# Kernel tuning notes

Measured on AMD Instinct MI355X. Metric: run time of the kernel, lower is better.

## Reference

```python
import jax, jax.numpy as jnp
import numpy as np

NUM_CLUSTERS = 512
EMBED_DIM = 256
BATCH = 65536
ALPHA = 0.05

def setup_inputs() -> dict:
    key = jax.random.key(0)
    k1, k2 = jax.random.split(key)
    embeddings = jax.random.normal(k1, (BATCH, EMBED_DIM), dtype=jnp.float32)
    # torch.randn centers drawn inside forward; materialized here for determinism
    centers = jax.random.normal(k2, (NUM_CLUSTERS, EMBED_DIM), dtype=jnp.float32)
    return {"embeddings": embeddings, "centers": centers}

def reference(embeddings, centers):
    # the broadcast difference, without the huge [N, K, D] intermediate).
    x_sq = jnp.sum(embeddings * embeddings, axis=1, keepdims=True)      # [N, 1]
    c_sq = jnp.sum(centers * centers, axis=1)[None, :]                  # [1, K]
    cross = embeddings @ centers.T                                      # [N, K]
    distances = jnp.sqrt(jnp.maximum(x_sq + c_sq - 2.0 * cross, 0.0))   # [N, K]
    cluster_assignments = jnp.argmin(distances, axis=1)                 # [N] int
    # gather distance to assigned (nearest) center
    cluster_loss = jnp.take_along_axis(
        distances, cluster_assignments[:, None], axis=1)[:, 0]          # [N]
    kmeans_loss = jnp.mean(cluster_loss)
    return kmeans_loss * ALPHA
```

## Files before the change

kernel.cpp:

```cpp
#include <hip/hip_runtime.h>
#include <hip/hip_bf16.h>

#define NROWS 65536
#define DIM   256
#define KC    512
#define ALPHA 0.05f

#define BM   64
#define SLD  264

typedef __attribute__((ext_vector_type(8))) short bf16x8;
typedef __attribute__((ext_vector_type(4))) float f32x4;

static __device__ __forceinline__ unsigned short f2bf(float f) {
    union { __hip_bfloat16 h; unsigned short u; } c;
    c.h = __float2bfloat16(f);
    return c.u;
}
static __device__ __forceinline__ float bf2f(unsigned short u) {
    union { unsigned short u; __hip_bfloat16 h; } c;
    c.u = u;
    return __bfloat162float(c.h);
}

__global__ void prep_centers(const float* __restrict__ centers,
                             float* __restrict__ csqh,
                             uint4* __restrict__ cbf2,
                             float* __restrict__ out) {
    const int t = threadIdx.x;
    const int r = blockIdx.x * 8 + (t >> 5);
    const int e = t & 31;
    const float4* cv = reinterpret_cast<const float4*>(centers);
    float4 v0 = cv[r * 64 + e * 2];
    float4 v1 = cv[r * 64 + e * 2 + 1];
    float s = v0.x * v0.x + v0.y * v0.y + v0.z * v0.z + v0.w * v0.w
            + v1.x * v1.x + v1.y * v1.y + v1.z * v1.z + v1.w * v1.w;
    unsigned short o[8];
    o[0] = f2bf(v0.x); o[1] = f2bf(v0.y); o[2] = f2bf(v0.z); o[3] = f2bf(v0.w);
    o[4] = f2bf(v1.x); o[5] = f2bf(v1.y); o[6] = f2bf(v1.z); o[7] = f2bf(v1.w);
    const int ch = r >> 6, w = (r >> 4) & 3, m = r & 15;
    const int kk = e >> 2, q = e & 3, l = q * 16 + m;
    cbf2[(((ch * 4 + w) * 8) + kk) * 64 + l] = *reinterpret_cast<uint4*>(o);
    #pragma unroll
    for (int off = 16; off; off >>= 1) s += __shfl_xor(s, off, 64);
    if (e == 0) csqh[r] = 0.5f * s;
    if (blockIdx.x == 0 && t == 0) out[0] = 0.f;
}

__global__ __launch_bounds__(256, 2) void kmeans_main(
    const float* __restrict__ emb,
    const uint4* __restrict__ cbf2,
    const float* __restrict__ csqh_g,
    float* __restrict__ out) {
    __shared__ unsigned short sA[BM * SLD];
    __shared__ float xsq_s[BM];
    __shared__ float rowmax_s[4][BM];

    const int t = threadIdx.x;
    const int w = t >> 6;
    const int lane = t & 63;
    const int m = lane & 15;
    const int q = lane >> 4;
    const int row0 = blockIdx.x * BM;

    const float4* embv = reinterpret_cast<const float4*>(emb + (size_t)row0 * DIM);
    #pragma unroll
    for (int i = 0; i < 16; ++i) {
        int f = t + 256 * i;
        int r = f >> 6;
        int c4 = f & 63;
        float4 v = embv[r * 64 + c4];
        ushort4 o;
        o.x = f2bf(v.x); o.y = f2bf(v.y); o.z = f2bf(v.z); o.w = f2bf(v.w);
        *reinterpret_cast<ushort4*>(&sA[r * SLD + c4 * 4]) = o;
    }
    __syncthreads();

    {
        int r = w * 16 + (lane >> 2);
        int qq = lane & 3;
        const ushort4* p = reinterpret_cast<const ushort4*>(&sA[r * SLD + qq * 64]);
        float s = 0.f;
        #pragma unroll
        for (int j = 0; j < 16; ++j) {
            ushort4 u = p[j];
            float a = bf2f(u.x), b = bf2f(u.y), c = bf2f(u.z), d = bf2f(u.w);
            s += a * a + b * b + c * c + d * d;
        }
        s += __shfl_xor(s, 1, 64);
        s += __shfl_xor(s, 2, 64);
        if (qq == 0) xsq_s[r] = s;
    }

    bf16x8 afr[4][8];
    #pragma unroll
    for (int rt = 0; rt < 4; ++rt)
        #pragma unroll
        for (int k = 0; k < 8; ++k)
            afr[rt][k] = *reinterpret_cast<const bf16x8*>(
                &sA[(rt * 16 + m) * SLD + k * 32 + q * 8]);

    float c2h[8];
    #pragma unroll
    for (int ch = 0; ch < 8; ++ch) c2h[ch] = csqh_g[ch * 64 + w * 16 + m];

    float maxv[4][4];
    #pragma unroll
    for (int rt = 0; rt < 4; ++rt)
        #pragma unroll
        for (int rg = 0; rg < 4; ++rg) maxv[rt][rg] = -1e30f;

    const bf16x8* cb2 = reinterpret_cast<const bf16x8*>(cbf2);

    bf16x8 bcur[8];
    #pragma unroll
    for (int kk = 0; kk < 8; ++kk)
        bcur[kk] = cb2[((0 * 4 + w) * 8 + kk) * 64 + lane];

    #pragma unroll
    for (int ch = 0; ch < 8; ++ch) {
        bf16x8 bnxt[8];
        if (ch < 7) {
            #pragma unroll
            for (int kk = 0; kk < 8; ++kk)
                bnxt[kk] = cb2[(((ch + 1) * 4 + w) * 8 + kk) * 64 + lane];
        }
        const float ci = -c2h[ch];
        f32x4 acc[4];
        #pragma unroll
        for (int rt = 0; rt < 4; ++rt) acc[rt] = (f32x4){ci, ci, ci, ci};
        #pragma unroll
        for (int kk = 0; kk < 8; ++kk)
            #pragma unroll
            for (int rt = 0; rt < 4; ++rt)
                acc[rt] = __builtin_amdgcn_mfma_f32_16x16x32_bf16(
                    afr[rt][kk], bcur[kk], acc[rt], 0, 0, 0);
        #pragma unroll
        for (int rt = 0; rt < 4; ++rt)
            #pragma unroll
            for (int rg = 0; rg < 4; ++rg)
                maxv[rt][rg] = fmaxf(maxv[rt][rg], acc[rt][rg]);
        if (ch < 7) {
            #pragma unroll
            for (int kk = 0; kk < 8; ++kk) bcur[kk] = bnxt[kk];
        }
    }

    #pragma unroll
    for (int rt = 0; rt < 4; ++rt)
        #pragma unroll
        for (int rg = 0; rg < 4; ++rg) {
            float v = maxv[rt][rg];
            v = fmaxf(v, __shfl_xor(v, 1, 64));
            v = fmaxf(v, __shfl_xor(v, 2, 64));
            v = fmaxf(v, __shfl_xor(v, 4, 64));
            v = fmaxf(v, __shfl_xor(v, 8, 64));
            if (m == 0) rowmax_s[w][rt * 16 + q * 4 + rg] = v;
        }
    __syncthreads();

    if (t < 64) {
        float M = fmaxf(fmaxf(rowmax_s[0][t], rowmax_s[1][t]),
                        fmaxf(rowmax_s[2][t], rowmax_s[3][t]));
        float d = sqrtf(fmaxf(xsq_s[t] - 2.f * M, 0.f));
        #pragma unroll
        for (int off = 1; off < 64; off <<= 1) d += __shfl_xor(d, off, 64);
        if (t == 0) atomicAdd(out, d * (ALPHA / (float)NROWS));
    }
}

extern "C" void kernel_launch(void* const* d_in, const int* in_sizes, int n_in,
                              void* d_out, int out_size, void* d_ws, size_t ws_size,
                              hipStream_t stream) {
    const float* emb     = (const float*)d_in[0];
    const float* centers = (const float*)d_in[1];
    float* out = (float*)d_out;

    float* csqh = (float*)d_ws;
    uint4* cbf2 = (uint4*)((char*)d_ws + 2048);

    prep_centers<<<dim3(KC / 8), dim3(256), 0, stream>>>(centers, csqh, cbf2, out);
    kmeans_main<<<dim3(NROWS / BM), dim3(256), 0, stream>>>(emb, cbf2, csqh, out);
}
```

Measured before the change: 118.9 us.

## Make kmeans blocks persistent over four tiles with double-buffered direct-to-LDS loads

Each block now handles four 64-row tiles instead of one. Embedding rows are staged as fp32 in two LDS buffers using global_load_lds DMA, and the next tile's rows are issued between MFMA chunks so global loads overlap compute. Conversion to bf16 and the squared-norm computation move to the fragment-load stage. Occupancy drops to one block per CU because fp32 double buffers use much more LDS, and the correctness of the manual waitcnt/barrier synchronisation is delicate.

```diff
diff --git a/kernel.cpp b/kernel.cpp
--- a/kernel.cpp
+++ b/kernel.cpp
@@ -6,8 +6,10 @@
 #define KC    512
 #define ALPHA 0.05f
 
-#define BM   64
-#define SLD  264
+#define BM    64
+#define NT    4
+#define GRID  (NROWS / (BM * NT))
+#define SROW  260
 
 typedef __attribute__((ext_vector_type(8))) short bf16x8;
 typedef __attribute__((ext_vector_type(4))) float f32x4;
@@ -47,126 +49,148 @@
     if (blockIdx.x == 0 && t == 0) out[0] = 0.f;
 }
 
-__global__ __launch_bounds__(256, 2) void kmeans_main(
+__global__ __launch_bounds__(256, 1) void kmeans_main(
     const float* __restrict__ emb,
     const uint4* __restrict__ cbf2,
     const float* __restrict__ csqh_g,
     float* __restrict__ out) {
-    __shared__ unsigned short sA[BM * SLD];
-    __shared__ float xsq_s[BM];
-    __shared__ float rowmax_s[4][BM];
+    __shared__ __align__(16) float fbuf[2][BM * SROW];
+    __shared__ float xsq_s[2][4][BM];
+    __shared__ float rowmax_s[2][4][BM];
 
     const int t = threadIdx.x;
     const int w = t >> 6;
     const int lane = t & 63;
     const int m = lane & 15;
     const int q = lane >> 4;
-    const int row0 = blockIdx.x * BM;
-
-    const float4* embv = reinterpret_cast<const float4*>(emb + (size_t)row0 * DIM);
-    #pragma unroll
-    for (int i = 0; i < 16; ++i) {
-        int f = t + 256 * i;
-        int r = f >> 6;
-        int c4 = f & 63;
-        float4 v = embv[r * 64 + c4];
-        ushort4 o;
-        o.x = f2bf(v.x); o.y = f2bf(v.y); o.z = f2bf(v.z); o.w = f2bf(v.w);
-        *reinterpret_cast<ushort4*>(&sA[r * SLD + c4 * 4]) = o;
+    const size_t block_row0 = (size_t)blockIdx.x * (BM * NT);
+
+    float c2h[8];
+    #pragma unroll
+    for (int ch = 0; ch < 8; ++ch) c2h[ch] = csqh_g[ch * 64 + w * 16 + m];
+
+    const bf16x8* cb2 = reinterpret_cast<const bf16x8*>(cbf2);
+
+#define DMA_ROW(tt_, bb_, rr_)                                                   \
+    do {                                                                         \
+        const float* g_ = emb +                                                  \
+            (block_row0 + (size_t)(tt_) * BM + (size_t)(rr_)) * DIM + (lane << 2); \
+        __builtin_amdgcn_global_load_lds(                                        \
+            (const __attribute__((address_space(1))) void*)g_,                   \
+            (__attribute__((address_space(3))) void*)&fbuf[bb_][(rr_) * SROW],   \
+            16, 0, 0);                                                           \
+    } while (0)
+
+    #pragma unroll
+    for (int j = 0; j < 16; ++j) DMA_ROW(0, 0, w * 16 + j);
+    #pragma unroll
+    for (int j = 0; j < 16; ++j) DMA_ROW(1, 1, w * 16 + j);
+    asm volatile("s_waitcnt vmcnt(16)\n\ts_barrier" ::: "memory");
+
+    for (int tt = 0; tt < NT; ++tt) {
+        const int p = tt & 1;
+        const bool dma_on = (tt + 2 < NT);
+
+        bf16x8 afr[4][8];
+        float xacc[4] = {0.f, 0.f, 0.f, 0.f};
+        #pragma unroll
+        for (int rt = 0; rt < 4; ++rt) {
+            const float* rp = &fbuf[p][(rt * 16 + m) * SROW + q * 8];
+            #pragma unroll
+            for (int kk = 0; kk < 8; ++kk) {
+                f32x4 v0 = *reinterpret_cast<const f32x4*>(rp + kk * 32);
+                f32x4 v1 = *reinterpret_cast<const f32x4*>(rp + kk * 32 + 4);
+                unsigned short o[8];
+                o[0] = f2bf(v0.x); o[1] = f2bf(v0.y); o[2] = f2bf(v0.z); o[3] = f2bf(v0.w);
+                o[4] = f2bf(v1.x); o[5] = f2bf(v1.y); o[6] = f2bf(v1.z); o[7] = f2bf(v1.w);
+                afr[rt][kk] = *reinterpret_cast<bf16x8*>(o);
+                if ((kk >> 1) == w) {
+                    #pragma unroll
+                    for (int j = 0; j < 8; ++j) { float f = bf2f(o[j]); xacc[rt] += f * f; }
+                }
+            }
+        }
+        #pragma unroll
+        for (int rt = 0; rt < 4; ++rt) {
+            float s = xacc[rt];
+            s += __shfl_xor(s, 16, 64);
+            s += __shfl_xor(s, 32, 64);
+            if (q == 0) xsq_s[p][w][rt * 16 + m] = s;
+        }
+
+        bf16x8 bcur[8];
+        #pragma unroll
+        for (int kk = 0; kk < 8; ++kk)
+            bcur[kk] = cb2[((0 * 4 + w) * 8 + kk) * 64 + lane];
+
+        asm volatile("s_waitcnt lgkmcnt(0)\n\ts_barrier" ::: "memory");
+
+        float maxv[4][4];
+        #pragma unroll
+        for (int rt = 0; rt < 4; ++rt)
+            #pragma unroll
+            for (int rg = 0; rg < 4; ++rg) maxv[rt][rg] = -1e30f;
+
+        #pragma unroll
+        for (int ch = 0; ch < 8; ++ch) {
+            if (dma_on) {
+                DMA_ROW(tt + 2, p, w * 16 + 2 * ch);
+                DMA_ROW(tt + 2, p, w * 16 + 2 * ch + 1);
+            }
+            bf16x8 bnxt[8];
+            if (ch < 7) {
+                #pragma unroll
+                for (int kk = 0; kk < 8; ++kk)
+                    bnxt[kk] = cb2[(((ch + 1) * 4 + w) * 8 + kk) * 64 + lane];
+            }
+            const float ci = -c2h[ch];
+            f32x4 acc[4];
+            #pragma unroll
+            for (int rt = 0; rt < 4; ++rt) acc[rt] = (f32x4){ci, ci, ci, ci};
+            #pragma unroll
+            for (int kk = 0; kk < 8; ++kk)
+                #pragma unroll
+                for (int rt = 0; rt < 4; ++rt)
+                    acc[rt] = __builtin_amdgcn_mfma_f32_16x16x32_bf16(
+                        afr[rt][kk], bcur[kk], acc[rt], 0, 0, 0);
+            #pragma unroll
+            for (int rt = 0; rt < 4; ++rt)
+                #pragma unroll
+                for (int rg = 0; rg < 4; ++rg)
+                    maxv[rt][rg] = fmaxf(maxv[rt][rg], acc[rt][rg]);
+            if (ch < 7) {
+                #pragma unroll
+                for (int kk = 0; kk < 8; ++kk) bcur[kk] = bnxt[kk];
+            }
+            __builtin_amdgcn_sched_barrier(0);
+        }
+
+        #pragma unroll
+        for (int rt = 0; rt < 4; ++rt)
+            #pragma unroll
+            for (int rg = 0; rg < 4; ++rg) {
+                float v = maxv[rt][rg];
+                v = fmaxf(v, __shfl_xor(v, 1, 64));
+                v = fmaxf(v, __shfl_xor(v, 2, 64));
+                v = fmaxf(v, __shfl_xor(v, 4, 64));
+                v = fmaxf(v, __shfl_xor(v, 8, 64));
+                if (m == 0) rowmax_s[p][w][rt * 16 + q * 4 + rg] = v;
+            }
+        asm volatile("s_waitcnt lgkmcnt(0)\n\ts_barrier" ::: "memory");
+
+        if (t < 64) {
+            float M = fmaxf(fmaxf(rowmax_s[p][0][t], rowmax_s[p][1][t]),
+                            fmaxf(rowmax_s[p][2][t], rowmax_s[p][3][t]));
+            float xs = xsq_s[p][0][t] + xsq_s[p][1][t]
+                     + xsq_s[p][2][t] + xsq_s[p][3][t];
+            float d = sqrtf(fmaxf(xs - 2.f * M, 0.f));
+            #pragma unroll
+            for (int off = 1; off < 64; off <<= 1) d += __shfl_xor(d, off, 64);
+            if (t == 0) atomicAdd(out, d * (ALPHA / (float)NROWS));
+        }
     }
-    __syncthreads();
-
-    {
-        int r = w * 16 + (lane >> 2);
-        int qq = lane & 3;
-        const ushort4* p = reinterpret_cast<const ushort4*>(&sA[r * SLD + qq * 64]);
-        float s = 0.f;
-        #pragma unroll
-        for (int j = 0; j < 16; ++j) {
-            ushort4 u = p[j];
-            float a = bf2f(u.x), b = bf2f(u.y), c = bf2f(u.z), d = bf2f(u.w);
-            s += a * a + b * b + c * c + d * d;
-        }
-        s += __shfl_xor(s, 1, 64);
-        s += __shfl_xor(s, 2, 64);
-        if (qq == 0) xsq_s[r] = s;
-    }
-
-    bf16x8 afr[4][8];
-    #pragma unroll
-    for (int rt = 0; rt < 4; ++rt)
-        #pragma unroll
-        for (int k = 0; k < 8; ++k)
-            afr[rt][k] = *reinterpret_cast<const bf16x8*>(
-                &sA[(rt * 16 + m) * SLD + k * 32 + q * 8]);
-
-    float c2h[8];
-    #pragma unroll
-    for (int ch = 0; ch < 8; ++ch) c2h[ch] = csqh_g[ch * 64 + w * 16 + m];
-
-    float maxv[4][4];
-    #pragma unroll
-    for (int rt = 0; rt < 4; ++rt)
-        #pragma unroll
-        for (int rg = 0; rg < 4; ++rg) maxv[rt][rg] = -1e30f;
-
-    const bf16x8* cb2 = reinterpret_cast<const bf16x8*>(cbf2);
-
-    bf16x8 bcur[8];
-    #pragma unroll
-    for (int kk = 0; kk < 8; ++kk)
-        bcur[kk] = cb2[((0 * 4 + w) * 8 + kk) * 64 + lane];
-
-    #pragma unroll
-    for (int ch = 0; ch < 8; ++ch) {
-        bf16x8 bnxt[8];
-        if (ch < 7) {
-            #pragma unroll
-            for (int kk = 0; kk < 8; ++kk)
-                bnxt[kk] = cb2[(((ch + 1) * 4 + w) * 8 + kk) * 64 + lane];
-        }
-        const float ci = -c2h[ch];
-        f32x4 acc[4];
-        #pragma unroll
-        for (int rt = 0; rt < 4; ++rt) acc[rt] = (f32x4){ci, ci, ci, ci};
-        #pragma unroll
-        for (int kk = 0; kk < 8; ++kk)
-            #pragma unroll
-            for (int rt = 0; rt < 4; ++rt)
-                acc[rt] = __builtin_amdgcn_mfma_f32_16x16x32_bf16(
-                    afr[rt][kk], bcur[kk], acc[rt], 0, 0, 0);
-        #pragma unroll
-        for (int rt = 0; rt < 4; ++rt)
-            #pragma unroll
-            for (int rg = 0; rg < 4; ++rg)
-                maxv[rt][rg] = fmaxf(maxv[rt][rg], acc[rt][rg]);
-        if (ch < 7) {
-            #pragma unroll
-            for (int kk = 0; kk < 8; ++kk) bcur[kk] = bnxt[kk];
-        }
-    }
-
-    #pragma unroll
-    for (int rt = 0; rt < 4; ++rt)
-        #pragma unroll
-        for (int rg = 0; rg < 4; ++rg) {
-            float v = maxv[rt][rg];
-            v = fmaxf(v, __shfl_xor(v, 1, 64));
-            v = fmaxf(v, __shfl_xor(v, 2, 64));
-            v = fmaxf(v, __shfl_xor(v, 4, 64));
-            v = fmaxf(v, __shfl_xor(v, 8, 64));
-            if (m == 0) rowmax_s[w][rt * 16 + q * 4 + rg] = v;
-        }
-    __syncthreads();
-
-    if (t < 64) {
-        float M = fmaxf(fmaxf(rowmax_s[0][t], rowmax_s[1][t]),
-                        fmaxf(rowmax_s[2][t], rowmax_s[3][t]));
-        float d = sqrtf(fmaxf(xsq_s[t] - 2.f * M, 0.f));
-        #pragma unroll
-        for (int off = 1; off < 64; off <<= 1) d += __shfl_xor(d, off, 64);
-        if (t == 0) atomicAdd(out, d * (ALPHA / (float)NROWS));
-    }
+    asm volatile("s_waitcnt vmcnt(0)" ::: "memory");
+#undef DMA_ROW
 }
 
 extern "C" void kernel_launch(void* const* d_in, const int* in_sizes, int n_in,
@@ -180,5 +204,5 @@
     uint4* cbf2 = (uint4*)((char*)d_ws + 2048);
 
     prep_centers<<<dim3(KC / 8), dim3(256), 0, stream>>>(centers, csqh, cbf2, out);
-    kmeans_main<<<dim3(NROWS / BM), dim3(256), 0, stream>>>(emb, cbf2, csqh, out);
-}
+    kmeans_main<<<dim3(GRID), dim3(256), 0, stream>>>(emb, cbf2, csqh, out);
+}
```

Measured after the change: 128.9 us. 8.4% more time.

## Load embeddings directly into registers and split block work 2x2 over rows and centers

Applied to the files above, without the earlier changes.

Removes the shared-memory staging of the embedding tile. Each lane now loads its own MFMA A-fragments straight from global memory and converts them to bf16 in registers, and only half the warps compute row norms. The 4 warps are rearranged as 2 row-halves by 2 center-halves, each covering 32 rows and 256 centers, so per-warp A fragments drop from 4 to 2 tiles. That frees registers, and launch bounds are raised to target 3 blocks per SM. In exchange each warp streams twice as many center chunks (16 iterations instead of 8), so the total center-fragment loads from L2 double. The global embedding loads are also less coalesced per lane.

```diff
diff --git a/kernel.cpp b/kernel.cpp
--- a/kernel.cpp
+++ b/kernel.cpp
@@ -5,9 +5,6 @@
 #define DIM   256
 #define KC    512
 #define ALPHA 0.05f
-
-#define BM   64
-#define SLD  264
 
 typedef __attribute__((ext_vector_type(8))) short bf16x8;
 typedef __attribute__((ext_vector_type(4))) float f32x4;
@@ -38,116 +35,110 @@
     unsigned short o[8];
     o[0] = f2bf(v0.x); o[1] = f2bf(v0.y); o[2] = f2bf(v0.z); o[3] = f2bf(v0.w);
     o[4] = f2bf(v1.x); o[5] = f2bf(v1.y); o[6] = f2bf(v1.z); o[7] = f2bf(v1.w);
-    const int ch = r >> 6, w = (r >> 4) & 3, m = r & 15;
+    const int cg = r >> 4, m = r & 15;
     const int kk = e >> 2, q = e & 3, l = q * 16 + m;
-    cbf2[(((ch * 4 + w) * 8) + kk) * 64 + l] = *reinterpret_cast<uint4*>(o);
+    cbf2[(cg * 8 + kk) * 64 + l] = *reinterpret_cast<uint4*>(o);
     #pragma unroll
     for (int off = 16; off; off >>= 1) s += __shfl_xor(s, off, 64);
     if (e == 0) csqh[r] = 0.5f * s;
     if (blockIdx.x == 0 && t == 0) out[0] = 0.f;
 }
 
-__global__ __launch_bounds__(256, 2) void kmeans_main(
+__global__ __launch_bounds__(256, 3) void kmeans_main(
     const float* __restrict__ emb,
     const uint4* __restrict__ cbf2,
     const float* __restrict__ csqh_g,
     float* __restrict__ out) {
-    __shared__ unsigned short sA[BM * SLD];
-    __shared__ float xsq_s[BM];
-    __shared__ float rowmax_s[4][BM];
+    __shared__ float lmax[4][32];
+    __shared__ float lx2[64];
 
     const int t = threadIdx.x;
     const int w = t >> 6;
     const int lane = t & 63;
     const int m = lane & 15;
     const int q = lane >> 4;
-    const int row0 = blockIdx.x * BM;
+    const int rowbase = blockIdx.x * 64 + (w >> 1) * 32;
+    const int cgbase  = (w & 1) * 16;
+    const bool do_x2  = (w & 1) == 0;
 
-    const float4* embv = reinterpret_cast<const float4*>(emb + (size_t)row0 * DIM);
+    bf16x8 afr[2][8];
+    float x2v[2];
     #pragma unroll
-    for (int i = 0; i < 16; ++i) {
-        int f = t + 256 * i;
-        int r = f >> 6;
-        int c4 = f & 63;
-        float4 v = embv[r * 64 + c4];
-        ushort4 o;
-        o.x = f2bf(v.x); o.y = f2bf(v.y); o.z = f2bf(v.z); o.w = f2bf(v.w);
-        *reinterpret_cast<ushort4*>(&sA[r * SLD + c4 * 4]) = o;
+    for (int rt = 0; rt < 2; ++rt) {
+        const float* rp = emb + (size_t)(rowbase + rt * 16 + m) * DIM + q * 8;
+        float xs = 0.f;
+        #pragma unroll
+        for (int kk = 0; kk < 8; ++kk) {
+            f32x4 v0 = *reinterpret_cast<const f32x4*>(rp + kk * 32);
+            f32x4 v1 = *reinterpret_cast<const f32x4*>(rp + kk * 32 + 4);
+            unsigned short o[8];
+            o[0] = f2bf(v0.x); o[1] = f2bf(v0.y); o[2] = f2bf(v0.z); o[3] = f2bf(v0.w);
+            o[4] = f2bf(v1.x); o[5] = f2bf(v1.y); o[6] = f2bf(v1.z); o[7] = f2bf(v1.w);
+            afr[rt][kk] = *reinterpret_cast<bf16x8*>(o);
+            if (do_x2) {
+                #pragma unroll
+                for (int j = 0; j < 8; ++j) { float f = bf2f(o[j]); xs += f * f; }
+            }
+        }
+        if (do_x2) {
+            xs += __shfl_xor(xs, 16, 64);
+            xs += __shfl_xor(xs, 32, 64);
+            x2v[rt] = xs;
+        }
+        __builtin_amdgcn_sched_barrier(0);
     }
-    __syncthreads();
-
-    {
-        int r = w * 16 + (lane >> 2);
-        int qq = lane & 3;
-        const ushort4* p = reinterpret_cast<const ushort4*>(&sA[r * SLD + qq * 64]);
-        float s = 0.f;
-        #pragma unroll
-        for (int j = 0; j < 16; ++j) {
-            ushort4 u = p[j];
-            float a = bf2f(u.x), b = bf2f(u.y), c = bf2f(u.z), d = bf2f(u.w);
-            s += a * a + b * b + c * c + d * d;
-        }
-        s += __shfl_xor(s, 1, 64);
-        s += __shfl_xor(s, 2, 64);
-        if (qq == 0) xsq_s[r] = s;
+    if (do_x2 && q == 0) {
+        lx2[(w >> 1) * 32 + m]      = x2v[0];
+        lx2[(w >> 1) * 32 + 16 + m] = x2v[1];
     }
 
-    bf16x8 afr[4][8];
+    const bf16x8* cb2 = reinterpret_cast<const bf16x8*>(cbf2);
+    float maxv[2][4];
     #pragma unroll
-    for (int rt = 0; rt < 4; ++rt)
-        #pragma unroll
-        for (int k = 0; k < 8; ++k)
-            afr[rt][k] = *reinterpret_cast<const bf16x8*>(
-                &sA[(rt * 16 + m) * SLD + k * 32 + q * 8]);
-
-    float c2h[8];
-    #pragma unroll
-    for (int ch = 0; ch < 8; ++ch) c2h[ch] = csqh_g[ch * 64 + w * 16 + m];
-
-    float maxv[4][4];
-    #pragma unroll
-    for (int rt = 0; rt < 4; ++rt)
+    for (int rt = 0; rt < 2; ++rt)
         #pragma unroll
         for (int rg = 0; rg < 4; ++rg) maxv[rt][rg] = -1e30f;
 
-    const bf16x8* cb2 = reinterpret_cast<const bf16x8*>(cbf2);
-
+    float c2cur = csqh_g[cgbase * 16 + m];
     bf16x8 bcur[8];
     #pragma unroll
     for (int kk = 0; kk < 8; ++kk)
-        bcur[kk] = cb2[((0 * 4 + w) * 8 + kk) * 64 + lane];
+        bcur[kk] = cb2[((cgbase + 0) * 8 + kk) * 64 + lane];
 
     #pragma unroll
-    for (int ch = 0; ch < 8; ++ch) {
+    for (int i = 0; i < 16; ++i) {
         bf16x8 bnxt[8];
-        if (ch < 7) {
+        float c2n = 0.f;
+        if (i < 15) {
+            c2n = csqh_g[(cgbase + i + 1) * 16 + m];
             #pragma unroll
             for (int kk = 0; kk < 8; ++kk)
-                bnxt[kk] = cb2[(((ch + 1) * 4 + w) * 8 + kk) * 64 + lane];
+                bnxt[kk] = cb2[((cgbase + i + 1) * 8 + kk) * 64 + lane];
         }
-        const float ci = -c2h[ch];
-        f32x4 acc[4];
-        #pragma unroll
-        for (int rt = 0; rt < 4; ++rt) acc[rt] = (f32x4){ci, ci, ci, ci};
+        const float ci = -c2cur;
+        f32x4 acc[2];
+        acc[0] = (f32x4){ci, ci, ci, ci};
+        acc[1] = (f32x4){ci, ci, ci, ci};
         #pragma unroll
         for (int kk = 0; kk < 8; ++kk)
             #pragma unroll
-            for (int rt = 0; rt < 4; ++rt)
+            for (int rt = 0; rt < 2; ++rt)
                 acc[rt] = __builtin_amdgcn_mfma_f32_16x16x32_bf16(
                     afr[rt][kk], bcur[kk], acc[rt], 0, 0, 0);
         #pragma unroll
-        for (int rt = 0; rt < 4; ++rt)
+        for (int rt = 0; rt < 2; ++rt)
             #pragma unroll
             for (int rg = 0; rg < 4; ++rg)
                 maxv[rt][rg] = fmaxf(maxv[rt][rg], acc[rt][rg]);
-        if (ch < 7) {
+        if (i < 15) {
             #pragma unroll
             for (int kk = 0; kk < 8; ++kk) bcur[kk] = bnxt[kk];
+            c2cur = c2n;
         }
     }
 
     #pragma unroll
-    for (int rt = 0; rt < 4; ++rt)
+    for (int rt = 0; rt < 2; ++rt)
         #pragma unroll
         for (int rg = 0; rg < 4; ++rg) {
             float v = maxv[rt][rg];
@@ -155,14 +146,15 @@
             v = fmaxf(v, __shfl_xor(v, 2, 64));
             v = fmaxf(v, __shfl_xor(v, 4, 64));
             v = fmaxf(v, __shfl_xor(v, 8, 64));
-            if (m == 0) rowmax_s[w][rt * 16 + q * 4 + rg] = v;
+            if (m == 0) lmax[w][rt * 16 + q * 4 + rg] = v;
         }
     __syncthreads();
 
     if (t < 64) {
-        float M = fmaxf(fmaxf(rowmax_s[0][t], rowmax_s[1][t]),
-                        fmaxf(rowmax_s[2][t], rowmax_s[3][t]));
-        float d = sqrtf(fmaxf(xsq_s[t] - 2.f * M, 0.f));
+        const int rg2 = t >> 5;
+        const int r = t & 31;
+        float M = fmaxf(lmax[rg2 * 2][r], lmax[rg2 * 2 + 1][r]);
+        float d = sqrtf(fmaxf(lx2[t] - 2.f * M, 0.f));
         #pragma unroll
         for (int off = 1; off < 64; off <<= 1) d += __shfl_xor(d, off, 64);
         if (t == 0) atomicAdd(out, d * (ALPHA / (float)NROWS));
@@ -180,5 +172,5 @@
     uint4* cbf2 = (uint4*)((char*)d_ws + 2048);
 
     prep_centers<<<dim3(KC / 8), dim3(256), 0, stream>>>(centers, csqh, cbf2, out);
-    kmeans_main<<<dim3(NROWS / BM), dim3(256), 0, stream>>>(emb, cbf2, csqh, out);
+    kmeans_main<<<dim3(NROWS / 64), dim3(256), 0, stream>>>(emb, cbf2, csqh, out);
 }
```

After: 159.8 us. 1.34x slower.

## Halve row tile to 32 and give each wave a contiguous 128-center slice

Applied to the files above, without the earlier changes.

The row tile drops from 64 to 32 per block, doubling the grid, and the launch bound asks for 3 blocks per CU instead of 2. The center layout is simplified to contiguous 16-center groups, so each wave now owns 128 consecutive centers, which the old interleaved 64-center chunking did not give it. The double-buffered prefetch of center fragments is removed in favour of loading inside the loop. This aims to improve occupancy and cut register pressure, but halves center-fragment reuse per load, so each embedding row now triggers twice as much center traffic from L2.

```diff
diff --git a/kernel.cpp b/kernel.cpp
--- a/kernel.cpp
+++ b/kernel.cpp
@@ -6,7 +6,7 @@
 #define KC    512
 #define ALPHA 0.05f
 
-#define BM   64
+#define BM   32
 #define SLD  264
 
 typedef __attribute__((ext_vector_type(8))) short bf16x8;
@@ -38,23 +38,23 @@
     unsigned short o[8];
     o[0] = f2bf(v0.x); o[1] = f2bf(v0.y); o[2] = f2bf(v0.z); o[3] = f2bf(v0.w);
     o[4] = f2bf(v1.x); o[5] = f2bf(v1.y); o[6] = f2bf(v1.z); o[7] = f2bf(v1.w);
-    const int ch = r >> 6, w = (r >> 4) & 3, m = r & 15;
+    const int cg = r >> 4, m = r & 15;
     const int kk = e >> 2, q = e & 3, l = q * 16 + m;
-    cbf2[(((ch * 4 + w) * 8) + kk) * 64 + l] = *reinterpret_cast<uint4*>(o);
+    cbf2[(cg * 8 + kk) * 64 + l] = *reinterpret_cast<uint4*>(o);
     #pragma unroll
     for (int off = 16; off; off >>= 1) s += __shfl_xor(s, off, 64);
     if (e == 0) csqh[r] = 0.5f * s;
     if (blockIdx.x == 0 && t == 0) out[0] = 0.f;
 }
 
-__global__ __launch_bounds__(256, 2) void kmeans_main(
+__global__ __launch_bounds__(256, 3) void kmeans_main(
     const float* __restrict__ emb,
     const uint4* __restrict__ cbf2,
     const float* __restrict__ csqh_g,
     float* __restrict__ out) {
     __shared__ unsigned short sA[BM * SLD];
-    __shared__ float xsq_s[BM];
-    __shared__ float rowmax_s[4][BM];
+    __shared__ float lmax[4][BM];
+    __shared__ float lx2[BM];
 
     const int t = threadIdx.x;
     const int w = t >> 6;
@@ -65,7 +65,7 @@
 
     const float4* embv = reinterpret_cast<const float4*>(emb + (size_t)row0 * DIM);
     #pragma unroll
-    for (int i = 0; i < 16; ++i) {
+    for (int i = 0; i < 8; ++i) {
         int f = t + 256 * i;
         int r = f >> 6;
         int c4 = f & 63;
@@ -77,77 +77,63 @@
     __syncthreads();
 
     {
-        int r = w * 16 + (lane >> 2);
-        int qq = lane & 3;
-        const ushort4* p = reinterpret_cast<const ushort4*>(&sA[r * SLD + qq * 64]);
+        int r = t >> 3;
+        int g = t & 7;
+        const ushort4* p = reinterpret_cast<const ushort4*>(&sA[r * SLD + g * 32]);
         float s = 0.f;
         #pragma unroll
-        for (int j = 0; j < 16; ++j) {
+        for (int j = 0; j < 8; ++j) {
             ushort4 u = p[j];
             float a = bf2f(u.x), b = bf2f(u.y), c = bf2f(u.z), d = bf2f(u.w);
             s += a * a + b * b + c * c + d * d;
         }
         s += __shfl_xor(s, 1, 64);
         s += __shfl_xor(s, 2, 64);
-        if (qq == 0) xsq_s[r] = s;
+        s += __shfl_xor(s, 4, 64);
+        if (g == 0) lx2[r] = s;
     }
 
-    bf16x8 afr[4][8];
+    bf16x8 afr[2][8];
     #pragma unroll
-    for (int rt = 0; rt < 4; ++rt)
+    for (int rt = 0; rt < 2; ++rt)
         #pragma unroll
         for (int k = 0; k < 8; ++k)
             afr[rt][k] = *reinterpret_cast<const bf16x8*>(
                 &sA[(rt * 16 + m) * SLD + k * 32 + q * 8]);
 
-    float c2h[8];
+    const bf16x8* cb2 = reinterpret_cast<const bf16x8*>(cbf2);
+    float maxv[2][4];
     #pragma unroll
-    for (int ch = 0; ch < 8; ++ch) c2h[ch] = csqh_g[ch * 64 + w * 16 + m];
-
-    float maxv[4][4];
-    #pragma unroll
-    for (int rt = 0; rt < 4; ++rt)
+    for (int rt = 0; rt < 2; ++rt)
         #pragma unroll
         for (int rg = 0; rg < 4; ++rg) maxv[rt][rg] = -1e30f;
 
-    const bf16x8* cb2 = reinterpret_cast<const bf16x8*>(cbf2);
-
-    bf16x8 bcur[8];
     #pragma unroll
-    for (int kk = 0; kk < 8; ++kk)
-        bcur[kk] = cb2[((0 * 4 + w) * 8 + kk) * 64 + lane];
-
-    #pragma unroll
-    for (int ch = 0; ch < 8; ++ch) {
-        bf16x8 bnxt[8];
-        if (ch < 7) {
-            #pragma unroll
-            for (int kk = 0; kk < 8; ++kk)
-                bnxt[kk] = cb2[(((ch + 1) * 4 + w) * 8 + kk) * 64 + lane];
-        }
-        const float ci = -c2h[ch];
-        f32x4 acc[4];
+    for (int cg = 0; cg < 8; ++cg) {
+        const int g = w * 8 + cg;
+        const float ci = -csqh_g[g * 16 + m];
+        bf16x8 bcur[8];
         #pragma unroll
-        for (int rt = 0; rt < 4; ++rt) acc[rt] = (f32x4){ci, ci, ci, ci};
+        for (int kk = 0; kk < 8; ++kk)
+            bcur[kk] = cb2[(g * 8 + kk) * 64 + lane];
+        f32x4 acc[2];
+        acc[0] = (f32x4){ci, ci, ci, ci};
+        acc[1] = (f32x4){ci, ci, ci, ci};
         #pragma unroll
         for (int kk = 0; kk < 8; ++kk)
             #pragma unroll
-            for (int rt = 0; rt < 4; ++rt)
+            for (int rt = 0; rt < 2; ++rt)
                 acc[rt] = __builtin_amdgcn_mfma_f32_16x16x32_bf16(
                     afr[rt][kk], bcur[kk], acc[rt], 0, 0, 0);
         #pragma unroll
-        for (int rt = 0; rt < 4; ++rt)
+        for (int rt = 0; rt < 2; ++rt)
             #pragma unroll
             for (int rg = 0; rg < 4; ++rg)
                 maxv[rt][rg] = fmaxf(maxv[rt][rg], acc[rt][rg]);
-        if (ch < 7) {
-            #pragma unroll
-            for (int kk = 0; kk < 8; ++kk) bcur[kk] = bnxt[kk];
-        }
     }
 
     #pragma unroll
-    for (int rt = 0; rt < 4; ++rt)
+    for (int rt = 0; rt < 2; ++rt)
         #pragma unroll
         for (int rg = 0; rg < 4; ++rg) {
             float v = maxv[rt][rg];
@@ -155,16 +141,16 @@
             v = fmaxf(v, __shfl_xor(v, 2, 64));
             v = fmaxf(v, __shfl_xor(v, 4, 64));
             v = fmaxf(v, __shfl_xor(v, 8, 64));
-            if (m == 0) rowmax_s[w][rt * 16 + q * 4 + rg] = v;
+            if (m == 0) lmax[w][rt * 16 + q * 4 + rg] = v;
         }
     __syncthreads();
 
-    if (t < 64) {
-        float M = fmaxf(fmaxf(rowmax_s[0][t], rowmax_s[1][t]),
-                        fmaxf(rowmax_s[2][t], rowmax_s[3][t]));
-        float d = sqrtf(fmaxf(xsq_s[t] - 2.f * M, 0.f));
+    if (t < 32) {
+        float M = fmaxf(fmaxf(lmax[0][t], lmax[1][t]),
+                        fmaxf(lmax[2][t], lmax[3][t]));
+        float d = sqrtf(fmaxf(lx2[t] - 2.f * M, 0.f));
         #pragma unroll
-        for (int off = 1; off < 64; off <<= 1) d += __shfl_xor(d, off, 64);
+        for (int off = 1; off < 32; off <<= 1) d += __shfl_xor(d, off, 64);
         if (t == 0) atomicAdd(out, d * (ALPHA / (float)NROWS));
     }
 }
```

New measurement: 125.0 us. 5.1% more time.
